# Kernel optimization log

Hardware: AMD Instinct MI355X
Metric: run time of the kernel (lower is better)

Reference implementation:

```python
import jax, jax.numpy as jnp
import numpy as np

B = 2
ROW, COL = 63, 84          # resolution
ROW_, COL_ = 32, 42        # resolution_
N = ROW * COL              # 5292 kv tokens
N_ = ROW_ * COL_           # 1344 q tokens
IN_DIM, OUT_DIM = 256, 512
KEY_DIM, NUM_HEADS, ATTN_RATIO, STRIDE = 16, 8, 2, 2
D = ATTN_RATIO * KEY_DIM   # 32 (value dim per head)
DH = D * NUM_HEADS         # 256
NH_KD = KEY_DIM * NUM_HEADS  # 128
H_KV = DH + NH_KD          # 384
SCALE = KEY_DIM ** -0.5
EPS = 1e-5


def _build_bias_idxs():
    # replicates the itertools.product double loop, vectorized; ids ordered by
    # first occurrence in row-major scan (same as dict insertion order).
    r_ = np.arange(ROW_); c_ = np.arange(COL_)
    r = np.arange(ROW); c = np.arange(COL)
    off_r = np.abs(r_[:, None] * STRIDE - r[None, :])      # (32, 63)
    off_c = np.abs(c_[:, None] * STRIDE - c[None, :])      # (42, 84)
    keys = (off_r[:, None, :, None] * 1000 + off_c[None, :, None, :]).reshape(-1)
    _, first_idx, inv = np.unique(keys, return_index=True, return_inverse=True)
    order = np.argsort(first_idx)
    rank = np.empty_like(order); rank[order] = np.arange(len(order))
    idxs = rank[inv].reshape(N_, N).astype(np.int32)
    return idxs, len(order)


def setup_inputs() -> dict:
    key = jax.random.key(0)
    ks = jax.random.split(key, 12)
    idxs_np, n_off = _build_bias_idxs()
    inp = {
        "x": jax.random.normal(ks[0], (B, N, IN_DIM), jnp.float32),
        "kv_w": jax.random.normal(ks[1], (H_KV, IN_DIM), jnp.float32) * (IN_DIM ** -0.5),
        "kv_g": jnp.ones((H_KV,), jnp.float32),
        "kv_b": jnp.zeros((H_KV,), jnp.float32),
        "q_w": jax.random.normal(ks[2], (NH_KD, IN_DIM), jnp.float32) * (IN_DIM ** -0.5),
        "q_g": jnp.ones((NH_KD,), jnp.float32),
        "q_b": jnp.zeros((NH_KD,), jnp.float32),
        "proj_w": jax.random.normal(ks[3], (OUT_DIM, DH), jnp.float32) * (DH ** -0.5),
        "proj_g": jnp.ones((OUT_DIM,), jnp.float32),
        "proj_b": jnp.zeros((OUT_DIM,), jnp.float32),
        "bias_table": jax.random.normal(ks[4], (NUM_HEADS, n_off), jnp.float32) * 0.02,
        "bias_idxs": jnp.asarray(idxs_np),
    }
    return inp


def _linear_bn(x, w, g, b):
    # Linear (no bias) followed by BatchNorm1d in training mode (batch stats
    # over flattened (B*N) dim, biased variance).
    y = jnp.einsum("bnc,oc->bno", x, w)
    flat = y.reshape(-1, y.shape[-1])
    mu = flat.mean(0)
    var = flat.var(0)
    return (y - mu) * (g / jnp.sqrt(var + EPS)) + b


def _hardswish(x):
    return x * jnp.clip(x + 3.0, 0.0, 6.0) / 6.0


def reference(x, kv_w, kv_g, kv_b, q_w, q_g, q_b, proj_w, proj_g, proj_b,
              bias_table, bias_idxs):
    Bx = x.shape[0]
    # kv projection -> split k (KEY_DIM) and v (D) per head
    kv = _linear_bn(x, kv_w, kv_g, kv_b).reshape(Bx, N, NUM_HEADS, KEY_DIM + D)
    k = kv[..., :KEY_DIM].transpose(0, 2, 1, 3)   # (B, H, N, key_dim)
    v = kv[..., KEY_DIM:].transpose(0, 2, 1, 3)   # (B, H, N, d)
    # q: spatial subsample then projection
    xs = x.reshape(Bx, ROW, COL, IN_DIM)[:, ::STRIDE, ::STRIDE].reshape(Bx, N_, IN_DIM)
    q = _linear_bn(xs, q_w, q_g, q_b).reshape(Bx, N_, NUM_HEADS, KEY_DIM).transpose(0, 2, 1, 3)
    # gathered relative position bias: (H, N_, N)
    ab = bias_table[:, bias_idxs]
    attn = jnp.einsum("bhqd,bhkd->bhqk", q, k) * SCALE + ab[None]
    attn = jax.nn.softmax(attn, axis=-1)
    out = jnp.einsum("bhqk,bhkd->bhqd", attn, v)       # (B, H, N_, d)
    out = out.transpose(0, 2, 1, 3).reshape(Bx, N_, DH)
    out = _linear_bn(_hardswish(out), proj_w, proj_g, proj_b)
    return out
```

## Files before the change

### kernel.cpp

```cpp
#include <hip/hip_runtime.h>
#include <hip/hip_bf16.h>
#include <math.h>

#define N_K 5292
#define N_KP 5376
#define N_Q 1344
#define NH_KD 128
#define NROWS 21504
#define LOG2E 1.4426950408889634f
#define MSTAT 16.0f

typedef float f32x4 __attribute__((ext_vector_type(4)));
typedef short short8 __attribute__((ext_vector_type(8)));

__device__ __forceinline__ float fexp2(float x) {
#if __has_builtin(__builtin_amdgcn_exp2f)
    return __builtin_amdgcn_exp2f(x);
#else
    return exp2f(x);
#endif
}

__device__ __forceinline__ unsigned pk_bf16(float a, float b) {
    union { __hip_bfloat162 h; unsigned u; } c;
    c.h = __float22bfloat162_rn(make_float2(a, b));
    return c.u;
}
__device__ __forceinline__ unsigned short f2bf(float a) {
    return (unsigned short)pk_bf16(a, 0.f);
}

__device__ __forceinline__ void gemm_body_f32(
    const float* __restrict__ A, const float* __restrict__ W,
    long asrc, int nrow,
    unsigned short (*As)[40], unsigned short (*Bs)[40], f32x4 acc[4])
{
    const int t = threadIdx.x;
    const int w = t >> 6, lane = t & 63, g = lane >> 4, ln = lane & 15;
    const int srow = t >> 2;
    const int sc8 = (t & 3) * 8;

    for (int k0 = 0; k0 < 256; k0 += 32) {
        uint4 a = make_uint4(0, 0, 0, 0);
        if (asrc >= 0) {
            float4 a0 = *(const float4*)(A + asrc * 256 + k0 + sc8);
            float4 a1 = *(const float4*)(A + asrc * 256 + k0 + sc8 + 4);
            a = make_uint4(pk_bf16(a0.x, a0.y), pk_bf16(a0.z, a0.w),
                           pk_bf16(a1.x, a1.y), pk_bf16(a1.z, a1.w));
        }
        float4 b0 = *(const float4*)(W + (size_t)nrow * 256 + k0 + sc8);
        float4 b1 = *(const float4*)(W + (size_t)nrow * 256 + k0 + sc8 + 4);
        uint4 b = make_uint4(pk_bf16(b0.x, b0.y), pk_bf16(b0.z, b0.w),
                             pk_bf16(b1.x, b1.y), pk_bf16(b1.z, b1.w));

        __syncthreads();
        *(uint4*)&As[srow][sc8] = a;
        *(uint4*)&Bs[srow][sc8] = b;
        __syncthreads();

        short8 ah = *(const short8*)&As[w * 16 + ln][g * 8];
        #pragma unroll
        for (int nt = 0; nt < 4; ++nt) {
            short8 bh = *(const short8*)&Bs[nt * 16 + ln][g * 8];
            acc[nt] = __builtin_amdgcn_mfma_f32_16x16x32_bf16(ah, bh, acc[nt], 0, 0, 0);
        }
    }
}

__device__ __forceinline__ void gemm_body_bf16(
    const unsigned short* __restrict__ A, const float* __restrict__ W,
    long asrc, int nrow,
    unsigned short (*As)[40], unsigned short (*Bs)[40], f32x4 acc[4])
{
    const int t = threadIdx.x;
    const int w = t >> 6, lane = t & 63, g = lane >> 4, ln = lane & 15;
    const int srow = t >> 2;
    const int sc8 = (t & 3) * 8;

    for (int k0 = 0; k0 < 256; k0 += 32) {
        uint4 a = *(const uint4*)(A + asrc * 256 + k0 + sc8);
        float4 b0 = *(const float4*)(W + (size_t)nrow * 256 + k0 + sc8);
        float4 b1 = *(const float4*)(W + (size_t)nrow * 256 + k0 + sc8 + 4);
        uint4 b = make_uint4(pk_bf16(b0.x, b0.y), pk_bf16(b0.z, b0.w),
                             pk_bf16(b1.x, b1.y), pk_bf16(b1.z, b1.w));

        __syncthreads();
        *(uint4*)&As[srow][sc8] = a;
        *(uint4*)&Bs[srow][sc8] = b;
        __syncthreads();

        short8 ah = *(const short8*)&As[w * 16 + ln][g * 8];
        #pragma unroll
        for (int nt = 0; nt < 4; ++nt) {
            short8 bh = *(const short8*)&Bs[nt * 16 + ln][g * 8];
            acc[nt] = __builtin_amdgcn_mfma_f32_16x16x32_bf16(ah, bh, acc[nt], 0, 0, 0);
        }
    }
}

__device__ __forceinline__ void gemm_stats(f32x4 acc[4], float* __restrict__ sums,
                                           int n0, int Ncols, float* scratch)
{
    const int t = threadIdx.x;
    const int w = t >> 6, lane = t & 63, g = lane >> 4, ln = lane & 15;
    float s4[4], q4[4];
    #pragma unroll
    for (int nt = 0; nt < 4; ++nt) {
        float s = acc[nt][0] + acc[nt][1] + acc[nt][2] + acc[nt][3];
        float q = fmaf(acc[nt][0], acc[nt][0], fmaf(acc[nt][1], acc[nt][1],
                  fmaf(acc[nt][2], acc[nt][2], acc[nt][3] * acc[nt][3])));
        s += __shfl_xor(s, 16); s += __shfl_xor(s, 32);
        q += __shfl_xor(q, 16); q += __shfl_xor(q, 32);
        s4[nt] = s; q4[nt] = q;
    }
    __syncthreads();
    float* st_s = scratch;
    float* st_q = scratch + 256;
    if (g == 0) {
        #pragma unroll
        for (int nt = 0; nt < 4; ++nt) {
            st_s[(w * 4 + nt) * 16 + ln] = s4[nt];
            st_q[(w * 4 + nt) * 16 + ln] = q4[nt];
        }
    }
    __syncthreads();
    if (t < 64) {
        int nt = t >> 4, c = t & 15;
        float a = 0.f, b2 = 0.f;
        #pragma unroll
        for (int ww = 0; ww < 4; ++ww) {
            a  += st_s[(ww * 4 + nt) * 16 + c];
            b2 += st_q[(ww * 4 + nt) * 16 + c];
        }
        atomicAdd(&sums[n0 + nt * 16 + c], a);
        atomicAdd(&sums[Ncols + n0 + nt * 16 + c], b2);
    }
}

__global__ __launch_bounds__(256) void gemm_qkv(
    const float* __restrict__ X, const float* __restrict__ kv_w, const float* __restrict__ q_w,
    const float* __restrict__ bias_table, const int* __restrict__ bias_idxs, int n_off,
    unsigned short* __restrict__ Kp, unsigned short* __restrict__ Vpt,
    float* __restrict__ bt_r,
    float* __restrict__ q_y, float* __restrict__ sums_kv, float* __restrict__ sums_q)
{
    __shared__ unsigned short As[64][40], Bs[64][40];
    const int t = threadIdx.x;
    const int w = t >> 6, lane = t & 63, g = lane >> 4, ln = lane & 15;
    const int srow = t >> 2;
    int id = blockIdx.x;

    if (id >= 1104) {
        id -= 1104;
        if (id < 168) {
            int i = id * 256 + t;
            int row = i / 84, j = i - row * 84;
            int slot;
            if (j < 20) {
                int kap = 44 + j;
                slot = 5248 + (((kap & 15) << 2) | (kap >> 4));
            } else {
                slot = 5312 + (j - 20);
            }
            Vpt[(size_t)row * N_KP + slot] = 0;
        } else {
            int i = (id - 168) * 256 + t;
            if (i < 8 * N_K) {
                int h = i / N_K, j = i - h * N_K;
                bt_r[i] = bias_table[h * n_off + bias_idxs[j]] * LOG2E;
            }
        }
        return;
    }

    f32x4 acc[4];
    #pragma unroll
    for (int nt = 0; nt < 4; ++nt) acc[nt] = (f32x4){0.f, 0.f, 0.f, 0.f};

    if (id < 1008) {
        const int xcd = id & 7, id8 = id >> 3;
        const int my = xcd + (id8 / 6) * 8, ny = id8 % 6;
        if (my >= 166) return;
        const int m0 = my * 64, n0 = ny * 64;
        int mrow = m0 + srow;
        long asrc = (mrow < 10584) ? mrow : -1;
        gemm_body_f32(X, kv_w, asrc, n0 + srow, As, Bs, acc);

        #pragma unroll
        for (int nt = 0; nt < 4; ++nt) {
            int c = n0 + nt * 16 + ln;
            int hh = c / 48, cc = c - 48 * hh;
            #pragma unroll
            for (int reg = 0; reg < 4; ++reg) {
                int mr = m0 + w * 16 + g * 4 + reg;
                if (mr < 10584) {
                    int bb = mr >= N_K;
                    int key = mr - bb * N_K;
                    unsigned short v16 = f2bf(acc[nt][reg]);
                    if (cc < 16) {
                        Kp[((size_t)(bb * 8 + hh) * N_K + key) * 16 + cc] = v16;
                    } else {
                        int kap = key & 63;
                        int keyp = (key & ~63) | (((kap & 15) << 2) | (kap >> 4));
                        Vpt[((size_t)(bb * 8 + hh) * 32 + cc - 16) * N_KP + keyp] = v16;
                    }
                }
            }
        }
        gemm_stats(acc, sums_kv, n0, 384, (float*)&As[0][0]);
    } else {
        id -= 1008;
        const int xcd = id & 7, id8 = id >> 3;
        const int my = xcd + (id8 / 2) * 8, ny = id8 % 2;
        if (my >= 42) return;
        const int m0 = my * 64, n0 = ny * 64;
        int mrow = m0 + srow;
        int bb = mrow / N_Q;
        int i = mrow - bb * N_Q;
        long asrc = (long)(bb * N_K + (i / 42) * 168 + (i % 42) * 2);
        gemm_body_f32(X, q_w, asrc, n0 + srow, As, Bs, acc);

        #pragma unroll
        for (int nt = 0; nt < 4; ++nt)
            #pragma unroll
            for (int reg = 0; reg < 4; ++reg) {
                int mr = m0 + w * 16 + g * 4 + reg;
                q_y[(size_t)mr * 128 + n0 + nt * 16 + ln] = acc[nt][reg];
            }
        gemm_stats(acc, sums_q, n0, 128, (float*)&As[0][0]);
    }
}

__global__ __launch_bounds__(256) void gemm_proj(
    const unsigned short* __restrict__ Ap, const float* __restrict__ Wp,
    float* __restrict__ Y, float* __restrict__ sums)
{
    __shared__ unsigned short As[64][40], Bs[64][40];
    const int t = threadIdx.x;
    const int w = t >> 6, lane = t & 63, g = lane >> 4, ln = lane & 15;
    const int id = blockIdx.x;
    const int xcd = id & 7, id8 = id >> 3;
    const int my = xcd + (id8 / 8) * 8, ny = id8 % 8;
    if (my >= 42) return;
    const int m0 = my * 64, n0 = ny * 64;

    f32x4 acc[4];
    #pragma unroll
    for (int nt = 0; nt < 4; ++nt) acc[nt] = (f32x4){0.f, 0.f, 0.f, 0.f};
    gemm_body_bf16(Ap, Wp, m0 + (t >> 2), n0 + (t >> 2), As, Bs, acc);

    #pragma unroll
    for (int nt = 0; nt < 4; ++nt)
        #pragma unroll
        for (int reg = 0; reg < 4; ++reg) {
            int mr = m0 + w * 16 + g * 4 + reg;
            Y[(size_t)mr * 512 + n0 + nt * 16 + ln] = acc[nt][reg];
        }
    gemm_stats(acc, sums, n0, 512, (float*)&As[0][0]);
}

__global__ __launch_bounds__(256, 5) void attn_mfma(
    const unsigned short* __restrict__ Kp, const unsigned short* __restrict__ Vpt,
    const float* __restrict__ q_y, const float* __restrict__ sums_q,
    const float* __restrict__ q_g, const float* __restrict__ q_b,
    const float* __restrict__ sums_kv, const float* __restrict__ kv_g,
    const float* __restrict__ bt_r,
    float* __restrict__ pl, float* __restrict__ pacc)
{
    const int id = blockIdx.x;
    const int h = id & 7;
    const int z = (id >> 3) & 7;
    const int qt = id >> 6;
    const int b = z >> 2, ks = z & 3;
    const int t = threadIdx.x;
    const int w = t >> 6, lane = t & 63, g = lane >> 4, ln = lane & 15;

    __shared__ unsigned short btm_s[21 * 166];
    __shared__ unsigned short K_s[2][64][24];
    __shared__ unsigned short Vt_s[2][32][72];
    __shared__ unsigned short P_s[4][16][72];

    const int q0 = qt * 64;
    const int kstart = ks * 1344;
    const int kend = (kstart + 1344 < N_K) ? kstart + 1344 : N_K;
    const int ntiles = (kend - kstart + 63) >> 6;
    const bool tail = (ks == 3);

    const int kr0 = kstart / 84;
    const int kr1 = (kend - 1) / 84;
    const int rq2min = (q0 / 42) * 2;
    const int rq2max = ((q0 + 63) / 42) * 2;
    const int dmin_r = rq2min - kr1;
    const int rows = (rq2max - kr0) - dmin_r + 1;
    const int nb = rows * 166;
    const int mx = nb - 1;
    {
        const float* src = bt_r + h * N_K;
        for (int j = t; j < nb; j += 256) {
            int rr = j / 166, ii = j - rr * 166;
            int dr = dmin_r + rr; dr = dr < 0 ? -dr : dr;
            int dc = ii - 83; dc = dc < 0 ? -dc : dc;
            btm_s[j] = f2bf(src[dr * 84 + dc]);
        }
    }

    short8 qfrag = (short8)0;
    if (lane < 32) {
        const float invq = 1.f / 2688.f, invk = 1.f / 10584.f;
        const float post = 0.25f * LOG2E;
        const int c0 = h * 16 + g * 8;
        const int ck = h * 48 + g * 8;
        const float* qp = q_y + (size_t)(b * N_Q + q0 + w * 16 + ln) * NH_KD + c0;
        float vv[8];
        #pragma unroll
        for (int j = 0; j < 8; ++j) {
            float mu  = sums_q[c0 + j] * invq;
            float var = fmaf(-mu, mu, sums_q[128 + c0 + j] * invq);
            float s   = q_g[c0 + j] * rsqrtf(var + 1e-5f) * post;
            float vq  = fmaf(qp[j], s, fmaf(-mu, s, q_b[c0 + j] * post));
            float muk = sums_kv[ck + j] * invk;
            float vrk = fmaf(-muk, muk, sums_kv[384 + ck + j] * invk);
            float sk  = kv_g[ck + j] * rsqrtf(vrk + 1e-5f);
            vv[j] = vq * sk;
        }
        union { short8 s; unsigned u[4]; } qf;
        qf.u[0] = pk_bf16(vv[0], vv[1]); qf.u[1] = pk_bf16(vv[2], vv[3]);
        qf.u[2] = pk_bf16(vv[4], vv[5]); qf.u[3] = pk_bf16(vv[6], vv[7]);
        qfrag = qf.s;
    }

    int base[4];
    #pragma unroll
    for (int reg = 0; reg < 4; ++reg) {
        int qg = q0 + w * 16 + g * 4 + reg;
        int rq2 = (qg / 42) * 2;
        int cq2 = (qg % 42) * 2;
        base[reg] = (rq2 - dmin_r) * 166 + cq2 + 83;
    }
    int off[4], kcc[4];
    #pragma unroll
    for (int st = 0; st < 4; ++st) {
        int kg = kstart + st * 16 + ln;
        int okr = kg / 84;
        kcc[st] = kg - okr * 84;
        off[st] = -(okr * 166 + kcc[st]);
    }

    const unsigned* kp_base = (const unsigned*)Kp + (size_t)(b * 8 + h) * N_K * 8;
    const unsigned short* vp_base = Vpt + (size_t)(b * 8 + h) * 32 * N_KP;
    const int skey = t >> 2, schunk = t & 3;
    const int vrow = t >> 3, vc8 = (t & 7) * 8;

    uint2 kreg; uint4 vreg;
    {
        int kg = kstart + skey; if (kg > N_K - 1) kg = N_K - 1;
        kreg = *(const uint2*)(kp_base + (size_t)kg * 8 + schunk * 2);
        vreg = *(const uint4*)(vp_base + (size_t)vrow * N_KP + kstart + vc8);
    }
    *(uint2*)&K_s[0][skey][schunk * 4] = kreg;
    *(uint4*)&Vt_s[0][vrow][vc8] = vreg;
    __syncthreads();

    float l[4] = {0.f, 0.f, 0.f, 0.f};
    f32x4 acc0 = {0.f, 0.f, 0.f, 0.f}, acc1 = {0.f, 0.f, 0.f, 0.f};
    const f32x4 minit = {-MSTAT, -MSTAT, -MSTAT, -MSTAT};
    int p = 0;

    for (int it = 0; it < ntiles; ++it) {
        const int k0 = kstart + it * 64;
        const bool notlast = (it + 1 < ntiles);
        if (notlast) {
            int kg = k0 + 64 + skey; if (kg > N_K - 1) kg = N_K - 1;
            kreg = *(const uint2*)(kp_base + (size_t)kg * 8 + schunk * 2);
            vreg = *(const uint4*)(vp_base + (size_t)vrow * N_KP + k0 + 64 + vc8);
        }

        f32x4 sf[4];
        #pragma unroll
        for (int st = 0; st < 4; ++st) {
            short8 bf = (short8)0;
            if (lane < 32) bf = *(const short8*)&K_s[p][st * 16 + ln][g * 8];
            sf[st] = __builtin_amdgcn_mfma_f32_16x16x32_bf16(qfrag, bf, minit, 0, 0, 0);
        }

        float pv[4][4];
        #pragma unroll
        for (int st = 0; st < 4; ++st) {
            #pragma unroll
            for (int reg = 0; reg < 4; ++reg) {
                int idx = base[reg] + off[st];
                idx = idx < 0 ? 0 : idx;
                idx = idx > mx ? mx : idx;
                float bias = __uint_as_float(((unsigned)btm_s[idx]) << 16);
                pv[st][reg] = fexp2(sf[st][reg] + bias);
            }
        }
        if (tail && it == ntiles - 1) {
            #pragma unroll
            for (int st = 0; st < 4; ++st) {
                bool bad = (k0 + st * 16 + ln) >= N_K;
                #pragma unroll
                for (int reg = 0; reg < 4; ++reg)
                    pv[st][reg] = bad ? 0.f : pv[st][reg];
            }
        }

        #pragma unroll
        for (int reg = 0; reg < 4; ++reg) {
            l[reg] += (pv[0][reg] + pv[1][reg]) + (pv[2][reg] + pv[3][reg]);
            uint2 pw = make_uint2(pk_bf16(pv[0][reg], pv[1][reg]),
                                  pk_bf16(pv[2][reg], pv[3][reg]));
            *(uint2*)&P_s[w][g * 4 + reg][4 * ln] = pw;
        }
        __asm__ __volatile__("" ::: "memory");

        #pragma unroll
        for (int kt = 0; kt < 2; ++kt) {
            short8 af = *(const short8*)&P_s[w][ln][g * 8 + kt * 32];
            short8 b0 = *(const short8*)&Vt_s[p][ln][g * 8 + kt * 32];
            short8 b1 = *(const short8*)&Vt_s[p][ln + 16][g * 8 + kt * 32];
            acc0 = __builtin_amdgcn_mfma_f32_16x16x32_bf16(af, b0, acc0, 0, 0, 0);
            acc1 = __builtin_amdgcn_mfma_f32_16x16x32_bf16(af, b1, acc1, 0, 0, 0);
        }

        if (notlast) {
            int q2 = p ^ 1;
            *(uint2*)&K_s[q2][skey][schunk * 4] = kreg;
            *(uint4*)&Vt_s[q2][vrow][vc8] = vreg;
            __syncthreads();
            p = q2;
        }

        #pragma unroll
        for (int st = 0; st < 4; ++st) {
            kcc[st] += 64;
            if (kcc[st] >= 84) { kcc[st] -= 84; off[st] -= 146; }
            else off[st] -= 64;
        }
    }

    #pragma unroll
    for (int reg = 0; reg < 4; ++reg) {
        float s = l[reg];
        s += __shfl_xor(s, 1, 16);
        s += __shfl_xor(s, 2, 16);
        s += __shfl_xor(s, 4, 16);
        s += __shfl_xor(s, 8, 16);
        l[reg] = s;
    }

    const int rbase = (b * 8 + h) * N_Q + q0 + w * 16;
    #pragma unroll
    for (int reg = 0; reg < 4; ++reg) {
        int prow = ks * NROWS + rbase + g * 4 + reg;
        pacc[(size_t)prow * 32 + ln]      = acc0[reg];
        pacc[(size_t)prow * 32 + 16 + ln] = acc1[reg];
        if (ln == 0) pl[prow] = l[reg];
    }
}

__global__ __launch_bounds__(256) void combine_kernel(const float* __restrict__ pl,
                                                      const float* __restrict__ pacc,
                                                      const float* __restrict__ sums_kv,
                                                      const float* __restrict__ kv_g,
                                                      const float* __restrict__ kv_b,
                                                      unsigned short* __restrict__ attn_o)
{
    int idx = blockIdx.x * 256 + threadIdx.x;
    int r = idx >> 3, e4 = (idx & 7) * 4;
    float L = (pl[r] + pl[NROWS + r]) + (pl[2 * NROWS + r] + pl[3 * NROWS + r]);
    float invL = 1.f / L;
    size_t o = (size_t)r * 32 + e4;
    float4 v0 = *(const float4*)(pacc + o);
    float4 v1 = *(const float4*)(pacc + (size_t)NROWS * 32 + o);
    float4 v2 = *(const float4*)(pacc + (size_t)2 * NROWS * 32 + o);
    float4 v3 = *(const float4*)(pacc + (size_t)3 * NROWS * 32 + o);
    int q = r % N_Q;
    int bh = r / N_Q;
    int hh = bh & 7, b = bh >> 3;
    const int ch = hh * 48 + 16 + e4;
    const float invk = 1.f / 10584.f;
    float hs[4];
    #pragma unroll
    for (int u = 0; u < 4; ++u) {
        float v = (u == 0 ? v0.x + v1.x + v2.x + v3.x :
                   u == 1 ? v0.y + v1.y + v2.y + v3.y :
                   u == 2 ? v0.z + v1.z + v2.z + v3.z :
                            v0.w + v1.w + v2.w + v3.w);
        float mu  = sums_kv[ch + u] * invk;
        float var = fmaf(-mu, mu, sums_kv[384 + ch + u] * invk);
        float s   = kv_g[ch + u] * rsqrtf(var + 1e-5f);
        float tt  = fmaf(-mu, s, kv_b[ch + u]);
        v = fmaf(s, v * invL, tt);
        hs[u] = v * fminf(fmaxf(v + 3.f, 0.f), 6.f) * (1.f / 6.f);
    }
    *(uint2*)(attn_o + (size_t)(b * N_Q + q) * 256 + hh * 32 + e4) =
        make_uint2(pk_bf16(hs[0], hs[1]), pk_bf16(hs[2], hs[3]));
}

__global__ __launch_bounds__(256) void norm_apply(
    const float* __restrict__ Y, const float* __restrict__ sums,
    const float* __restrict__ g, const float* __restrict__ bb,
    float* __restrict__ out, int rows, int cols, float inv_rows)
{
    __shared__ float sc_s[64], sh_s[64];
    const int t = threadIdx.x;
    const int c0 = blockIdx.x * 64;
    if (t < 64) {
        int c = c0 + t;
        float mu  = sums[c] * inv_rows;
        float var = fmaf(-mu, mu, sums[cols + c] * inv_rows);
        float s   = g[c] * rsqrtf(var + 1e-5f);
        sc_s[t] = s;
        sh_s[t] = fmaf(-mu, s, bb[c]);
    }
    __syncthreads();
    const int c4 = (t & 15) * 4;
    float4 scv = *(const float4*)&sc_s[c4];
    float4 shv = *(const float4*)&sh_s[c4];
    for (int r = blockIdx.y * 16 + (t >> 4); r < rows; r += gridDim.y * 16) {
        size_t off = (size_t)r * cols + c0 + c4;
        float4 v = *(const float4*)(Y + off);
        v.x = fmaf(v.x, scv.x, shv.x);
        v.y = fmaf(v.y, scv.y, shv.y);
        v.z = fmaf(v.z, scv.z, shv.z);
        v.w = fmaf(v.w, scv.w, shv.w);
        *(float4*)(out + off) = v;
    }
}

extern "C" void kernel_launch(void* const* d_in, const int* in_sizes, int n_in,
                              void* d_out, int out_size, void* d_ws, size_t ws_size,
                              hipStream_t stream) {
    (void)n_in; (void)out_size; (void)ws_size;
    const float* x      = (const float*)d_in[0];
    const float* kv_w   = (const float*)d_in[1];
    const float* kv_g   = (const float*)d_in[2];
    const float* kv_b   = (const float*)d_in[3];
    const float* q_w    = (const float*)d_in[4];
    const float* q_g    = (const float*)d_in[5];
    const float* q_b    = (const float*)d_in[6];
    const float* proj_w = (const float*)d_in[7];
    const float* proj_g = (const float*)d_in[8];
    const float* proj_b = (const float*)d_in[9];
    const float* bias_table = (const float*)d_in[10];
    const int*   bias_idxs  = (const int*)d_in[11];
    const int    n_off = in_sizes[10] / 8;
    float* out = (float*)d_out;

    float* ws = (float*)d_ws;
    float* q_y  = ws;
    float* pacc = q_y + 2688 * 128;
    float* proj_y = pacc;
    float* pl = pacc + 4 * NROWS * 32;
    unsigned short* attn_o = (unsigned short*)(pl + 4 * NROWS);
    unsigned short* Kp  = attn_o + 2688 * 256;
    unsigned short* Vpt = Kp + 2 * 8 * N_K * 16;
    float* sums_kv = (float*)(Vpt + 2 * 8 * 32 * N_KP);
    float* sums_q  = sums_kv + 768;
    float* sums_p  = sums_q + 256;
    float* bt_r    = sums_p + 1024;

    hipMemsetAsync(sums_kv, 0, 2048 * sizeof(float), stream);
    gemm_qkv<<<1104 + 168 + 166, 256, 0, stream>>>(x, kv_w, q_w, bias_table, bias_idxs,
                                                   n_off, Kp, Vpt, bt_r,
                                                   q_y, sums_kv, sums_q);
    attn_mfma<<<1344, 256, 0, stream>>>(Kp, Vpt, q_y, sums_q, q_g, q_b,
                                        sums_kv, kv_g, bt_r, pl, pacc);
    combine_kernel<<<672, 256, 0, stream>>>(pl, pacc, sums_kv, kv_g, kv_b, attn_o);
    gemm_proj<<<384, 256, 0, stream>>>(attn_o, proj_w, proj_y, sums_p);
    norm_apply<<<dim3(8, 84), 256, 0, stream>>>(proj_y, sums_p, proj_g, proj_b, out,
                                                2688, 512, 1.f / 2688.f);
}
```

Measured before the change: 198.4 us.

## Pre-convert inputs and weights to bf16 and streamline bias lookup in attention

Adds a prep kernel that converts x, kv_w and q_w to bf16 into workspace once. The QKV GEMMs then load bf16 directly instead of converting fp32 in every tile, and the same happens for proj_w, converted in extra blocks of the combine kernel. The attention loop switches to byte offsets with a single unsigned clamp for the bias lookup and accumulates the row sum as a packed float2. This adds one kernel launch and an extra read/write pass over x, while halving the GEMM operand traffic and removing repeated conversions.

```diff
diff --git a/kernel.cpp b/kernel.cpp
--- a/kernel.cpp
+++ b/kernel.cpp
@@ -11,6 +11,7 @@
 #define MSTAT 16.0f
 
 typedef float f32x4 __attribute__((ext_vector_type(4)));
+typedef float f32x2 __attribute__((ext_vector_type(2)));
 typedef short short8 __attribute__((ext_vector_type(8)));
 
 __device__ __forceinline__ float fexp2(float x) {
@@ -30,8 +31,24 @@
     return (unsigned short)pk_bf16(a, 0.f);
 }
 
-__device__ __forceinline__ void gemm_body_f32(
-    const float* __restrict__ A, const float* __restrict__ W,
+__global__ __launch_bounds__(256) void prep_bf16(
+    const float* __restrict__ X, const float* __restrict__ kv_w,
+    const float* __restrict__ q_w,
+    unsigned short* __restrict__ Xb)
+{
+    int i = blockIdx.x * 256 + threadIdx.x;
+    const float* src;
+    long off;
+    if (i < 677376)       { src = X;      off = i; }
+    else if (i < 701952)  { src = kv_w;   off = i - 677376; }
+    else if (i < 710144)  { src = q_w;    off = i - 701952; }
+    else return;
+    float4 v = *(const float4*)(src + off * 4);
+    *(uint2*)(Xb + (size_t)i * 4) = make_uint2(pk_bf16(v.x, v.y), pk_bf16(v.z, v.w));
+}
+
+__device__ __forceinline__ void gemm_body_bb(
+    const unsigned short* __restrict__ A, const unsigned short* __restrict__ W,
     long asrc, int nrow,
     unsigned short (*As)[40], unsigned short (*Bs)[40], f32x4 acc[4])
 {
@@ -42,47 +59,8 @@
 
     for (int k0 = 0; k0 < 256; k0 += 32) {
         uint4 a = make_uint4(0, 0, 0, 0);
-        if (asrc >= 0) {
-            float4 a0 = *(const float4*)(A + asrc * 256 + k0 + sc8);
-            float4 a1 = *(const float4*)(A + asrc * 256 + k0 + sc8 + 4);
-            a = make_uint4(pk_bf16(a0.x, a0.y), pk_bf16(a0.z, a0.w),
-                           pk_bf16(a1.x, a1.y), pk_bf16(a1.z, a1.w));
-        }
-        float4 b0 = *(const float4*)(W + (size_t)nrow * 256 + k0 + sc8);
-        float4 b1 = *(const float4*)(W + (size_t)nrow * 256 + k0 + sc8 + 4);
-        uint4 b = make_uint4(pk_bf16(b0.x, b0.y), pk_bf16(b0.z, b0.w),
-                             pk_bf16(b1.x, b1.y), pk_bf16(b1.z, b1.w));
-
-        __syncthreads();
-        *(uint4*)&As[srow][sc8] = a;
-        *(uint4*)&Bs[srow][sc8] = b;
-        __syncthreads();
-
-        short8 ah = *(const short8*)&As[w * 16 + ln][g * 8];
-        #pragma unroll
-        for (int nt = 0; nt < 4; ++nt) {
-            short8 bh = *(const short8*)&Bs[nt * 16 + ln][g * 8];
-            acc[nt] = __builtin_amdgcn_mfma_f32_16x16x32_bf16(ah, bh, acc[nt], 0, 0, 0);
-        }
-    }
-}
-
-__device__ __forceinline__ void gemm_body_bf16(
-    const unsigned short* __restrict__ A, const float* __restrict__ W,
-    long asrc, int nrow,
-    unsigned short (*As)[40], unsigned short (*Bs)[40], f32x4 acc[4])
-{
-    const int t = threadIdx.x;
-    const int w = t >> 6, lane = t & 63, g = lane >> 4, ln = lane & 15;
-    const int srow = t >> 2;
-    const int sc8 = (t & 3) * 8;
-
-    for (int k0 = 0; k0 < 256; k0 += 32) {
-        uint4 a = *(const uint4*)(A + asrc * 256 + k0 + sc8);
-        float4 b0 = *(const float4*)(W + (size_t)nrow * 256 + k0 + sc8);
-        float4 b1 = *(const float4*)(W + (size_t)nrow * 256 + k0 + sc8 + 4);
-        uint4 b = make_uint4(pk_bf16(b0.x, b0.y), pk_bf16(b0.z, b0.w),
-                             pk_bf16(b1.x, b1.y), pk_bf16(b1.z, b1.w));
+        if (asrc >= 0) a = *(const uint4*)(A + asrc * 256 + k0 + sc8);
+        uint4 b = *(const uint4*)(W + (size_t)nrow * 256 + k0 + sc8);
 
         __syncthreads();
         *(uint4*)&As[srow][sc8] = a;
@@ -138,7 +116,8 @@
 }
 
 __global__ __launch_bounds__(256) void gemm_qkv(
-    const float* __restrict__ X, const float* __restrict__ kv_w, const float* __restrict__ q_w,
+    const unsigned short* __restrict__ Xb, const unsigned short* __restrict__ kvWb,
+    const unsigned short* __restrict__ qWb,
     const float* __restrict__ bias_table, const int* __restrict__ bias_idxs, int n_off,
     unsigned short* __restrict__ Kp, unsigned short* __restrict__ Vpt,
     float* __restrict__ bt_r,
@@ -184,7 +163,7 @@
         const int m0 = my * 64, n0 = ny * 64;
         int mrow = m0 + srow;
         long asrc = (mrow < 10584) ? mrow : -1;
-        gemm_body_f32(X, kv_w, asrc, n0 + srow, As, Bs, acc);
+        gemm_body_bb(Xb, kvWb, asrc, n0 + srow, As, Bs, acc);
 
         #pragma unroll
         for (int nt = 0; nt < 4; ++nt) {
@@ -218,7 +197,7 @@
         int bb = mrow / N_Q;
         int i = mrow - bb * N_Q;
         long asrc = (long)(bb * N_K + (i / 42) * 168 + (i % 42) * 2);
-        gemm_body_f32(X, q_w, asrc, n0 + srow, As, Bs, acc);
+        gemm_body_bb(Xb, qWb, asrc, n0 + srow, As, Bs, acc);
 
         #pragma unroll
         for (int nt = 0; nt < 4; ++nt)
@@ -232,7 +211,7 @@
 }
 
 __global__ __launch_bounds__(256) void gemm_proj(
-    const unsigned short* __restrict__ Ap, const float* __restrict__ Wp,
+    const unsigned short* __restrict__ Ap, const unsigned short* __restrict__ Wp,
     float* __restrict__ Y, float* __restrict__ sums)
 {
     __shared__ unsigned short As[64][40], Bs[64][40];
@@ -247,7 +226,7 @@
     f32x4 acc[4];
     #pragma unroll
     for (int nt = 0; nt < 4; ++nt) acc[nt] = (f32x4){0.f, 0.f, 0.f, 0.f};
-    gemm_body_bf16(Ap, Wp, m0 + (t >> 2), n0 + (t >> 2), As, Bs, acc);
+    gemm_body_bb(Ap, Wp, m0 + (t >> 2), n0 + (t >> 2), As, Bs, acc);
 
     #pragma unroll
     for (int nt = 0; nt < 4; ++nt)
@@ -293,7 +272,7 @@
     const int dmin_r = rq2min - kr1;
     const int rows = (rq2max - kr0) - dmin_r + 1;
     const int nb = rows * 166;
-    const int mx = nb - 1;
+    const unsigned mxb = (unsigned)((nb - 1) * 2);
     {
         const float* src = bt_r + h * N_K;
         for (int j = t; j < nb; j += 256) {
@@ -329,21 +308,21 @@
         qfrag = qf.s;
     }
 
-    int base[4];
+    int baseb[4];
     #pragma unroll
     for (int reg = 0; reg < 4; ++reg) {
         int qg = q0 + w * 16 + g * 4 + reg;
         int rq2 = (qg / 42) * 2;
         int cq2 = (qg % 42) * 2;
-        base[reg] = (rq2 - dmin_r) * 166 + cq2 + 83;
-    }
-    int off[4], kcc[4];
+        baseb[reg] = ((rq2 - dmin_r) * 166 + cq2 + 83) * 2;
+    }
+    int offb[4], kcc[4];
     #pragma unroll
     for (int st = 0; st < 4; ++st) {
         int kg = kstart + st * 16 + ln;
         int okr = kg / 84;
         kcc[st] = kg - okr * 84;
-        off[st] = -(okr * 166 + kcc[st]);
+        offb[st] = -(okr * 166 + kcc[st]) * 2;
     }
 
     const unsigned* kp_base = (const unsigned*)Kp + (size_t)(b * 8 + h) * N_K * 8;
@@ -361,7 +340,9 @@
     *(uint4*)&Vt_s[0][vrow][vc8] = vreg;
     __syncthreads();
 
-    float l[4] = {0.f, 0.f, 0.f, 0.f};
+    f32x2 l2[4];
+    #pragma unroll
+    for (int reg = 0; reg < 4; ++reg) l2[reg] = (f32x2){0.f, 0.f};
     f32x4 acc0 = {0.f, 0.f, 0.f, 0.f}, acc1 = {0.f, 0.f, 0.f, 0.f};
     const f32x4 minit = {-MSTAT, -MSTAT, -MSTAT, -MSTAT};
     int p = 0;
@@ -388,10 +369,10 @@
         for (int st = 0; st < 4; ++st) {
             #pragma unroll
             for (int reg = 0; reg < 4; ++reg) {
-                int idx = base[reg] + off[st];
-                idx = idx < 0 ? 0 : idx;
-                idx = idx > mx ? mx : idx;
-                float bias = __uint_as_float(((unsigned)btm_s[idx]) << 16);
+                unsigned ub = (unsigned)(baseb[reg] + offb[st]);
+                ub = ub > mxb ? mxb : ub;
+                unsigned short bu = *(const unsigned short*)((const char*)btm_s + ub);
+                float bias = __uint_as_float(((unsigned)bu) << 16);
                 pv[st][reg] = fexp2(sf[st][reg] + bias);
             }
         }
@@ -407,7 +388,7 @@
 
         #pragma unroll
         for (int reg = 0; reg < 4; ++reg) {
-            l[reg] += (pv[0][reg] + pv[1][reg]) + (pv[2][reg] + pv[3][reg]);
+            l2[reg] += (f32x2){pv[0][reg], pv[2][reg]} + (f32x2){pv[1][reg], pv[3][reg]};
             uint2 pw = make_uint2(pk_bf16(pv[0][reg], pv[1][reg]),
                                   pk_bf16(pv[2][reg], pv[3][reg]));
             *(uint2*)&P_s[w][g * 4 + reg][4 * ln] = pw;
@@ -434,14 +415,15 @@
         #pragma unroll
         for (int st = 0; st < 4; ++st) {
             kcc[st] += 64;
-            if (kcc[st] >= 84) { kcc[st] -= 84; off[st] -= 146; }
-            else off[st] -= 64;
-        }
-    }
-
+            if (kcc[st] >= 84) { kcc[st] -= 84; offb[st] -= 292; }
+            else offb[st] -= 128;
+        }
+    }
+
+    float l[4];
     #pragma unroll
     for (int reg = 0; reg < 4; ++reg) {
-        float s = l[reg];
+        float s = l2[reg][0] + l2[reg][1];
         s += __shfl_xor(s, 1, 16);
         s += __shfl_xor(s, 2, 16);
         s += __shfl_xor(s, 4, 16);
@@ -464,8 +446,16 @@
                                                       const float* __restrict__ sums_kv,
                                                       const float* __restrict__ kv_g,
                                                       const float* __restrict__ kv_b,
-                                                      unsigned short* __restrict__ attn_o)
-{
+                                                      unsigned short* __restrict__ attn_o,
+                                                      const float* __restrict__ proj_w,
+                                                      unsigned short* __restrict__ projWb)
+{
+    if (blockIdx.x >= 672) {
+        int i = (blockIdx.x - 672) * 256 + threadIdx.x;
+        float4 v = *(const float4*)(proj_w + (size_t)i * 4);
+        *(uint2*)(projWb + (size_t)i * 4) = make_uint2(pk_bf16(v.x, v.y), pk_bf16(v.z, v.w));
+        return;
+    }
     int idx = blockIdx.x * 256 + threadIdx.x;
     int r = idx >> 3, e4 = (idx & 7) * 4;
     float L = (pl[r] + pl[NROWS + r]) + (pl[2 * NROWS + r] + pl[3 * NROWS + r]);
@@ -561,14 +551,21 @@
     float* sums_p  = sums_q + 256;
     float* bt_r    = sums_p + 1024;
 
+    unsigned short* Xb     = (unsigned short*)pacc;
+    unsigned short* kvWb   = Xb + 10584 * 256;
+    unsigned short* qWb    = kvWb + 384 * 256;
+    unsigned short* projWb = (unsigned short*)q_y;
+
     hipMemsetAsync(sums_kv, 0, 2048 * sizeof(float), stream);
-    gemm_qkv<<<1104 + 168 + 166, 256, 0, stream>>>(x, kv_w, q_w, bias_table, bias_idxs,
+    prep_bf16<<<2774, 256, 0, stream>>>(x, kv_w, q_w, Xb);
+    gemm_qkv<<<1104 + 168 + 166, 256, 0, stream>>>(Xb, kvWb, qWb, bias_table, bias_idxs,
                                                    n_off, Kp, Vpt, bt_r,
                                                    q_y, sums_kv, sums_q);
     attn_mfma<<<1344, 256, 0, stream>>>(Kp, Vpt, q_y, sums_q, q_g, q_b,
                                         sums_kv, kv_g, bt_r, pl, pacc);
-    combine_kernel<<<672, 256, 0, stream>>>(pl, pacc, sums_kv, kv_g, kv_b, attn_o);
-    gemm_proj<<<384, 256, 0, stream>>>(attn_o, proj_w, proj_y, sums_p);
+    combine_kernel<<<672 + 128, 256, 0, stream>>>(pl, pacc, sums_kv, kv_g, kv_b, attn_o,
+                                                  proj_w, projWb);
+    gemm_proj<<<384, 256, 0, stream>>>(attn_o, projWb, proj_y, sums_p);
     norm_apply<<<dim3(8, 84), 256, 0, stream>>>(proj_y, sums_p, proj_g, proj_b, out,
                                                 2688, 512, 1.f / 2688.f);
 }
```

Result: faster. 191.7 us (-3.4%).
